# Kernel optimization log

Measured on AMD Instinct MI355X. Metric: run time of the kernel, lower is better.

## Reference

```python
import jax, jax.numpy as jnp
import numpy as np

N, C, H, W = 8, 512, 64, 64
C8, C2 = C // 8, C // 2  # 64, 256


def _maxpool2(x):
    # 2x2 max pool, stride 2. x: [n, c, h, w] -> [n, c, h//2, w//2]
    n, c, h, w = x.shape
    return x.reshape(n, c, h // 2, 2, w // 2, 2).max(axis=(3, 5))


def setup_inputs() -> dict:
    key = jax.random.key(0)
    ks = jax.random.split(key, 6)
    s = lambda fan_in: 1.0 / np.sqrt(fan_in)
    return {
        "x": jax.random.normal(ks[0], (N, C, H, W), dtype=jnp.float32),
        "theta_w": jax.random.normal(ks[1], (C8, C), dtype=jnp.float32) * s(C),
        "theta_b": jnp.zeros((C8,), dtype=jnp.float32),
        "phi_w": jax.random.normal(ks[2], (C8, C), dtype=jnp.float32) * s(C),
        "phi_b": jnp.zeros((C8,), dtype=jnp.float32),
        "g_w": jax.random.normal(ks[3], (C2, C), dtype=jnp.float32) * s(C),
        "g_b": jnp.zeros((C2,), dtype=jnp.float32),
        "out_w": jax.random.normal(ks[4], (C, C2), dtype=jnp.float32) * s(C2),
        "out_b": jnp.zeros((C,), dtype=jnp.float32),
        "gamma": jnp.ones((1,), dtype=jnp.float32),
    }


def reference(x, theta_w, theta_b, phi_w, phi_b, g_w, g_b, out_w, out_b, gamma):
    n, c, h, w = x.shape
    hw, hw4 = h * w, (h * w) // 4

    # 1x1 convs == per-pixel matmuls over channels
    theta = jnp.einsum('nchw,kc->nkhw', x, theta_w) + theta_b[None, :, None, None]
    phi = jnp.einsum('nchw,kc->nkhw', x, phi_w) + phi_b[None, :, None, None]
    g = jnp.einsum('nchw,kc->nkhw', x, g_w) + g_b[None, :, None, None]

    theta = theta.reshape(n, -1, hw).transpose(0, 2, 1)        # [n, hw, c/8]
    phi = _maxpool2(phi).reshape(n, -1, hw4)                    # [n, c/8, hw/4]
    g = _maxpool2(g).reshape(n, -1, hw4)                        # [n, c/2, hw/4]

    energy = jnp.einsum('nqk,nkp->nqp', theta, phi)             # [n, hw, hw/4]
    attention = jax.nn.softmax(energy, axis=-1)

    out = jnp.einsum('ncp,nqp->ncq', g, attention)              # [n, c/2, hw]
    out = out.reshape(n, c // 2, h, w)
    out = jnp.einsum('nchw,kc->nkhw', out, out_w) + out_b[None, :, None, None]
    return gamma[0] * out + x
```

## Files before the change

kernel.cpp:

```cpp
#include <hip/hip_runtime.h>
#include <hip/hip_bf16.h>
#include <cmath>
#include <cstdint>

#define NB 8
#define HW 4096
#define PP 1024
#define C2 256

typedef _Float16 half_t;
typedef _Float16 half8 __attribute__((ext_vector_type(8)));
typedef _Float16 half4 __attribute__((ext_vector_type(4)));
typedef _Float16 half2t __attribute__((ext_vector_type(2)));
typedef float f32x4 __attribute__((ext_vector_type(4)));

__global__ __launch_bounds__(256) void prep_k(
    const float* __restrict__ tw, const float* __restrict__ pw,
    const float* __restrict__ gw, const float* __restrict__ ow,
    half_t* __restrict__ W16,
    const float* __restrict__ x, half_t* __restrict__ x16t)
{
    const int tid = threadIdx.x;
    const int bx = blockIdx.x;

    if (bx < 160) {
        int gid = bx * 256 + tid;
        size_t i0 = (size_t)gid * 8;
        const float* src; size_t off;
        if (i0 < 32768)       { src = tw; off = i0; }
        else if (i0 < 65536)  { src = pw; off = i0 - 32768; }
        else if (i0 < 196608) { src = gw; off = i0 - 65536; }
        else                  { src = ow; off = i0 - 196608; }
        float4 a = *(const float4*)&src[off];
        float4 b = *(const float4*)&src[off + 4];
        half8 h;
        h[0] = (half_t)a.x; h[1] = (half_t)a.y; h[2] = (half_t)a.z; h[3] = (half_t)a.w;
        h[4] = (half_t)b.x; h[5] = (half_t)b.y; h[6] = (half_t)b.z; h[7] = (half_t)b.w;
        *(half8*)&W16[i0] = h;
        return;
    }

    __shared__ half_t U[64][68];
    const int b = bx - 160;
    const int n  = b >> 9;
    const int bxx = b & 511;
    const int c0 = (bxx & 7) * 64;
    const int p0 = (bxx >> 3) * 64;

#pragma unroll
    for (int it = 0; it < 4; ++it) {
        int c = (tid >> 4) + 16 * it;
        int p4 = (tid & 15) * 4;
        float4 v = *(const float4*)&x[((size_t)n * 512 + c0 + c) * HW + p0 + p4];
        half4 h;
        h[0] = (half_t)v.x; h[1] = (half_t)v.y;
        h[2] = (half_t)v.z; h[3] = (half_t)v.w;
        *(half4*)&U[c][p4] = h;
    }
    __syncthreads();
#pragma unroll
    for (int it = 0; it < 2; ++it) {
        int p = (tid >> 3) + 32 * it;
        int ch = (tid & 7) * 8;
        half8 o;
#pragma unroll
        for (int j = 0; j < 8; ++j) o[j] = U[ch + j][p];
        *(half8*)&x16t[((size_t)n * HW + p0 + p) * 512 + c0 + ch] = o;
    }
}

#define SWZ(row, chunk) (((row) << 6) + ((((chunk) ^ ((row) & 7))) << 3))

__global__ __launch_bounds__(256, 3) void proj_k(
    const half_t* __restrict__ W16, const float* __restrict__ theta_b,
    const float* __restrict__ phi_b, const float* __restrict__ g_b,
    const half_t* __restrict__ x16t, half_t* __restrict__ theta16,
    half_t* __restrict__ phi16, half_t* __restrict__ g16)
{
    __shared__ __align__(16) char smem[36864];
    half_t* As = (half_t*)smem;
    half_t* Bs = (half_t*)(smem + 16384);

    const int tid = threadIdx.x;
    const int wave = tid >> 6, lane = tid & 63;
    const int quad = lane >> 4, lq = lane & 15;
    const int wn = (wave & 1) * 64, wm = (wave >> 1) * 64;
    const int n = blockIdx.z;
    const int p0 = blockIdx.x * 128;
    const int ysel = blockIdx.y;

    const half_t* A16 = (ysel == 0) ? W16
                        : (W16 + 65536 + (size_t)(ysel - 1) * 128 * 512);

    const int sr  = lane >> 3;
    const int scl = lane & 7;
    const int scg = scl ^ sr;

    f32x4 acc[4][4];
#pragma unroll
    for (int mt = 0; mt < 4; ++mt)
#pragma unroll
        for (int nt = 0; nt < 4; ++nt)
            acc[mt][nt] = (f32x4){0.f, 0.f, 0.f, 0.f};

    for (int c0 = 0; c0 < 512; c0 += 64) {
#pragma unroll
        for (int i = 0; i < 4; ++i) {
            int rb = (wave << 5) + (i << 3);
            int r = rb + sr;
            __builtin_amdgcn_global_load_lds(
                (const __attribute__((address_space(1))) uint32_t*)
                    &A16[(size_t)r * 512 + c0 + scg * 8],
                (__attribute__((address_space(3))) uint32_t*)&As[rb * 64],
                16, 0, 0);
        }
#pragma unroll
        for (int i = 0; i < 4; ++i) {
            int rb = (wave << 5) + (i << 3);
            int r = rb + sr;
            __builtin_amdgcn_global_load_lds(
                (const __attribute__((address_space(1))) uint32_t*)
                    &x16t[((size_t)n * HW + p0 + r) * 512 + c0 + scg * 8],
                (__attribute__((address_space(3))) uint32_t*)&Bs[rb * 64],
                16, 0, 0);
        }
        __syncthreads();
#pragma unroll
        for (int ks = 0; ks < 2; ++ks) {
            half8 af[4], bf[4];
#pragma unroll
            for (int mt = 0; mt < 4; ++mt)
                af[mt] = *(const half8*)&As[SWZ(wm + mt * 16 + lq, ks * 4 + quad)];
#pragma unroll
            for (int nt = 0; nt < 4; ++nt)
                bf[nt] = *(const half8*)&Bs[SWZ(wn + nt * 16 + lq, ks * 4 + quad)];
#pragma unroll
            for (int mt = 0; mt < 4; ++mt)
#pragma unroll
                for (int nt = 0; nt < 4; ++nt)
                    acc[mt][nt] = __builtin_amdgcn_mfma_f32_16x16x32_f16(
                        af[mt], bf[nt], acc[mt][nt], 0, 0, 0);
        }
        __syncthreads();
    }

    if (ysel == 0) {
        half_t* Cs = (half_t*)smem;
        if (wm == 0) {
#pragma unroll
            for (int mt = 0; mt < 4; ++mt) {
                float4 bv = *(const float4*)&theta_b[mt * 16 + quad * 4];
#pragma unroll
                for (int nt = 0; nt < 4; ++nt) {
                    int q = p0 + wn + nt * 16 + lq;
                    half4 h;
                    h[0] = (half_t)(acc[mt][nt][0] + bv.x);
                    h[1] = (half_t)(acc[mt][nt][1] + bv.y);
                    h[2] = (half_t)(acc[mt][nt][2] + bv.z);
                    h[3] = (half_t)(acc[mt][nt][3] + bv.w);
                    *(half4*)&theta16[((size_t)n * HW + q) * 64 + mt * 16 + quad * 4] = h;
                }
            }
        } else {
#pragma unroll
            for (int mt = 0; mt < 4; ++mt) {
                float4 bv = *(const float4*)&phi_b[mt * 16 + quad * 4];
#pragma unroll
                for (int nt = 0; nt < 4; ++nt) {
                    int col = wn + nt * 16 + lq;
                    int mr = mt * 16 + quad * 4;
                    Cs[(mr + 0) * 136 + col] = (half_t)(acc[mt][nt][0] + bv.x);
                    Cs[(mr + 1) * 136 + col] = (half_t)(acc[mt][nt][1] + bv.y);
                    Cs[(mr + 2) * 136 + col] = (half_t)(acc[mt][nt][2] + bv.z);
                    Cs[(mr + 3) * 136 + col] = (half_t)(acc[mt][nt][3] + bv.w);
                }
            }
        }
        __syncthreads();
        {
            int pw = tid >> 3;
            int kc = (tid & 7) * 8;
            half8 o;
#pragma unroll
            for (int jj = 0; jj < 8; ++jj) {
                int k = kc + jj;
                float v0 = (float)Cs[k * 136 + 2 * pw];
                float v1 = (float)Cs[k * 136 + 2 * pw + 1];
                float v2 = (float)Cs[k * 136 + 64 + 2 * pw];
                float v3 = (float)Cs[k * 136 + 65 + 2 * pw];
                o[jj] = (half_t)fmaxf(fmaxf(v0, v1), fmaxf(v2, v3));
            }
            *(half8*)&phi16[((size_t)n * PP + (p0 >> 7) * 32 + pw) * 64 + kc] = o;
        }
    } else {
        const int m0 = (ysel - 1) * 128;
        half_t* Cs = (half_t*)smem;
#pragma unroll
        for (int mt = 0; mt < 4; ++mt) {
            float4 bv = *(const float4*)&g_b[m0 + wm + mt * 16 + quad * 4];
#pragma unroll
            for (int nt = 0; nt < 4; ++nt) {
                int col = wn + nt * 16 + lq;
                int mr = wm + mt * 16 + quad * 4;
                Cs[(mr + 0) * 136 + col] = (half_t)(acc[mt][nt][0] + bv.x);
                Cs[(mr + 1) * 136 + col] = (half_t)(acc[mt][nt][1] + bv.y);
                Cs[(mr + 2) * 136 + col] = (half_t)(acc[mt][nt][2] + bv.z);
                Cs[(mr + 3) * 136 + col] = (half_t)(acc[mt][nt][3] + bv.w);
            }
        }
        __syncthreads();
#pragma unroll
        for (int i = 0; i < 16; ++i) {
            int m = (tid >> 5) + 8 * i;
            int pw = tid & 31;
            float v0 = (float)Cs[m * 136 + 2 * pw];
            float v1 = (float)Cs[m * 136 + 2 * pw + 1];
            float v2 = (float)Cs[m * 136 + 64 + 2 * pw];
            float v3 = (float)Cs[m * 136 + 65 + 2 * pw];
            g16[((size_t)n * C2 + m0 + m) * PP + (p0 >> 7) * 32 + pw] =
                (half_t)fmaxf(fmaxf(v0, v1), fmaxf(v2, v3));
        }
    }
}

__global__ __launch_bounds__(256, 2) void attn_fused_k(
    const half_t* __restrict__ theta16,
    const half_t* __restrict__ phi16,
    const half_t* __restrict__ g16,
    const half_t* __restrict__ W16o,
    const float* __restrict__ out_b,
    const float* __restrict__ x,
    const float* __restrict__ gam,
    float* __restrict__ outF)
{
    __shared__ half_t P[64][264];
    __shared__ float redM[4][64];
    __shared__ float redS[4][64];
    __shared__ float Ms[64], alpha_s[64], l_s[64], inv_s[64];

    const int tid  = threadIdx.x;
    const int wave = tid >> 6;
    const int lane = tid & 63;
    const int quad = lane >> 4;
    const int lq   = lane & 15;
    const int n  = blockIdx.y;
    const int q0 = blockIdx.x * 64;
    const int cb = wave * 64;

    const half_t* thN  = theta16 + ((size_t)n * HW + q0) * 64;
    const half_t* phiN = phi16 + (size_t)n * PP * 64;
    const half_t* gN   = g16 + (size_t)n * C2 * PP;

    if (tid < 64) { Ms[tid] = -1e30f; l_s[tid] = 0.f; }

    f32x4 acc[4][4];
#pragma unroll
    for (int ct = 0; ct < 4; ++ct)
#pragma unroll
        for (int qt = 0; qt < 4; ++qt)
            acc[ct][qt] = (f32x4){0.f, 0.f, 0.f, 0.f};

    for (int chunk = 0; chunk < 4; ++chunk) {
        const int pch = chunk * 256;

        half8 tb[4][2];
#pragma unroll
        for (int qt = 0; qt < 4; ++qt)
#pragma unroll
            for (int kb = 0; kb < 2; ++kb)
                tb[qt][kb] = *(const half8*)&thN[(size_t)(qt * 16 + lq) * 64 + kb * 32 + quad * 8];

        float mreg[4] = {-1e30f, -1e30f, -1e30f, -1e30f};
#pragma unroll
        for (int pt = 0; pt < 4; ++pt) {
            int pl = wave * 64 + pt * 16;
            const half_t* pr = &phiN[(size_t)(pch + pl + lq) * 64];
            half8 a0 = *(const half8*)&pr[quad * 8];
            half8 a1 = *(const half8*)&pr[32 + quad * 8];
#pragma unroll
            for (int qt = 0; qt < 4; ++qt) {
                f32x4 c = {0.f, 0.f, 0.f, 0.f};
                c = __builtin_amdgcn_mfma_f32_16x16x32_f16(a0, tb[qt][0], c, 0, 0, 0);
                c = __builtin_amdgcn_mfma_f32_16x16x32_f16(a1, tb[qt][1], c, 0, 0, 0);
                mreg[qt] = fmaxf(mreg[qt], fmaxf(fmaxf(c[0], c[1]), fmaxf(c[2], c[3])));
                half2t h0; h0[0] = (half_t)c[0]; h0[1] = (half_t)c[1];
                half2t h1; h1[0] = (half_t)c[2]; h1[1] = (half_t)c[3];
                *(half2t*)&P[qt * 16 + lq][pl + quad * 4]     = h0;
                *(half2t*)&P[qt * 16 + lq][pl + quad * 4 + 2] = h1;
            }
        }
#pragma unroll
        for (int qt = 0; qt < 4; ++qt) {
            float m = mreg[qt];
            m = fmaxf(m, __shfl_xor(m, 16));
            m = fmaxf(m, __shfl_xor(m, 32));
            mreg[qt] = m;
        }
        if (quad == 0) {
#pragma unroll
            for (int qt = 0; qt < 4; ++qt) redM[wave][qt * 16 + lq] = mreg[qt];
        }
        __syncthreads();

        if (tid < 64) {
            float cm = fmaxf(fmaxf(redM[0][tid], redM[1][tid]),
                             fmaxf(redM[2][tid], redM[3][tid]));
            float Mo = Ms[tid];
            float Mn = fmaxf(Mo, cm);
            alpha_s[tid] = __expf(Mo - Mn);
            Ms[tid] = Mn;
        }
        __syncthreads();

        {
            float al[4];
#pragma unroll
            for (int qt = 0; qt < 4; ++qt) al[qt] = alpha_s[qt * 16 + lq];
#pragma unroll
            for (int ct = 0; ct < 4; ++ct)
#pragma unroll
                for (int qt = 0; qt < 4; ++qt)
#pragma unroll
                    for (int r = 0; r < 4; ++r) acc[ct][qt][r] *= al[qt];
        }

        {
            int q = tid & 63, seg = tid >> 6;
            float M = Ms[q];
            float s = 0.f;
#pragma unroll
            for (int j = 0; j < 8; ++j) {
                half8 v = *(const half8*)&P[q][seg * 64 + j * 8];
                half8 o;
#pragma unroll
                for (int e = 0; e < 8; ++e) {
                    float f = __expf((float)v[e] - M);
                    s += f;
                    o[e] = (half_t)f;
                }
                *(half8*)&P[q][seg * 64 + j * 8] = o;
            }
            redS[seg][q] = s;
        }
        __syncthreads();

        if (tid < 64)
            l_s[tid] = l_s[tid] * alpha_s[tid]
                     + redS[0][tid] + redS[1][tid] + redS[2][tid] + redS[3][tid];

#pragma unroll
        for (int kb = 0; kb < 8; ++kb) {
            half8 b[4];
#pragma unroll
            for (int qt = 0; qt < 4; ++qt)
                b[qt] = *(const half8*)&P[qt * 16 + lq][kb * 32 + quad * 8];
#pragma unroll
            for (int ct = 0; ct < 4; ++ct) {
                half8 a = *(const half8*)&gN[(size_t)(cb + ct * 16 + lq) * PP + pch + kb * 32 + quad * 8];
#pragma unroll
                for (int qt = 0; qt < 4; ++qt)
                    acc[ct][qt] = __builtin_amdgcn_mfma_f32_16x16x32_f16(a, b[qt], acc[ct][qt], 0, 0, 0);
            }
        }
        __syncthreads();
    }

    if (tid < 64) inv_s[tid] = 1.0f / l_s[tid];
    __syncthreads();

    {
        float iv[4];
#pragma unroll
        for (int qt = 0; qt < 4; ++qt) iv[qt] = inv_s[qt * 16 + lq];
#pragma unroll
        for (int ct = 0; ct < 4; ++ct) {
#pragma unroll
            for (int qt = 0; qt < 4; ++qt) {
                half2t h0, h1;
                h0[0] = (half_t)(acc[ct][qt][0] * iv[qt]);
                h0[1] = (half_t)(acc[ct][qt][1] * iv[qt]);
                h1[0] = (half_t)(acc[ct][qt][2] * iv[qt]);
                h1[1] = (half_t)(acc[ct][qt][3] * iv[qt]);
                *(half2t*)&P[qt * 16 + lq][cb + ct * 16 + quad * 4]     = h0;
                *(half2t*)&P[qt * 16 + lq][cb + ct * 16 + quad * 4 + 2] = h1;
            }
        }
    }
    __syncthreads();

    const float g0 = gam[0];
#pragma unroll
    for (int pass = 0; pass < 2; ++pass) {
        const int mb = pass * 256 + wave * 64;
        f32x4 acc2[4][4];
#pragma unroll
        for (int mt = 0; mt < 4; ++mt)
#pragma unroll
            for (int qt = 0; qt < 4; ++qt)
                acc2[mt][qt] = (f32x4){0.f, 0.f, 0.f, 0.f};

#pragma unroll
        for (int kb = 0; kb < 8; ++kb) {
            half8 b[4];
#pragma unroll
            for (int qt = 0; qt < 4; ++qt)
                b[qt] = *(const half8*)&P[qt * 16 + lq][kb * 32 + quad * 8];
#pragma unroll
            for (int mt = 0; mt < 4; ++mt) {
                half8 a = *(const half8*)&W16o[(size_t)(mb + mt * 16 + lq) * 256 + kb * 32 + quad * 8];
#pragma unroll
                for (int qt = 0; qt < 4; ++qt)
                    acc2[mt][qt] = __builtin_amdgcn_mfma_f32_16x16x32_f16(a, b[qt], acc2[mt][qt], 0, 0, 0);
            }
        }

#pragma unroll
        for (int mt = 0; mt < 4; ++mt) {
            float4 bv = *(const float4*)&out_b[mb + mt * 16 + quad * 4];
#pragma unroll
            for (int qt = 0; qt < 4; ++qt) {
                int qg = q0 + qt * 16 + lq;
                int m = mb + mt * 16 + quad * 4;
                size_t off = ((size_t)(n * 512 + m)) * HW + qg;
                outF[off]          = g0 * (acc2[mt][qt][0] + bv.x) + x[off];
                outF[off + HW]     = g0 * (acc2[mt][qt][1] + bv.y) + x[off + HW];
                outF[off + 2*HW]   = g0 * (acc2[mt][qt][2] + bv.z) + x[off + 2*HW];
                outF[off + 3*HW]   = g0 * (acc2[mt][qt][3] + bv.w) + x[off + 3*HW];
            }
        }
    }
}

extern "C" void kernel_launch(void* const* d_in, const int* in_sizes, int n_in,
                              void* d_out, int out_size, void* d_ws, size_t ws_size,
                              hipStream_t stream)
{
    const float* x       = (const float*)d_in[0];
    const float* theta_w = (const float*)d_in[1];
    const float* theta_b = (const float*)d_in[2];
    const float* phi_w   = (const float*)d_in[3];
    const float* phi_b   = (const float*)d_in[4];
    const float* g_w     = (const float*)d_in[5];
    const float* g_b     = (const float*)d_in[6];
    const float* out_w   = (const float*)d_in[7];
    const float* out_b   = (const float*)d_in[8];
    const float* gamma   = (const float*)d_in[9];
    float* out = (float*)d_out;

    char* wsb = (char*)d_ws;
    half_t* x16t    = (half_t*)wsb;
    half_t* W16     = (half_t*)(wsb + 33554432);
    half_t* theta16 = (half_t*)(wsb + 34209792);
    half_t* phi16   = (half_t*)(wsb + 38404096);
    half_t* g16     = (half_t*)(wsb + 39452672);

    prep_k<<<160 + 512 * NB, 256, 0, stream>>>(
        theta_w, phi_w, g_w, out_w, W16, x, x16t);
    proj_k<<<dim3(32, 3, NB), 256, 0, stream>>>(
        W16, theta_b, phi_b, g_b, x16t, theta16, phi16, g16);
    attn_fused_k<<<dim3(HW / 64, NB), 256, 0, stream>>>(
        theta16, phi16, g16, W16 + 196608, out_b, x, gamma, out);
}
```

Baseline: 218.1 us.

## Swizzle prep transpose tile, flatten grids with batch-interleaved block order

New measurement: 213.8 us, median of 2. -2.0%, faster.

```diff
diff --git a/kernel.cpp b/kernel.cpp
--- a/kernel.cpp
+++ b/kernel.cpp
@@ -40,9 +40,9 @@
         return;
     }
 
-    __shared__ half_t U[64][68];
+    __shared__ half_t T[64][72];
     const int b = bx - 160;
-    const int n  = b >> 9;
+    const int n   = b >> 9;
     const int bxx = b & 511;
     const int c0 = (bxx & 7) * 64;
     const int p0 = (bxx >> 3) * 64;
@@ -52,26 +52,28 @@
         int c = (tid >> 4) + 16 * it;
         int p4 = (tid & 15) * 4;
         float4 v = *(const float4*)&x[((size_t)n * 512 + c0 + c) * HW + p0 + p4];
-        half4 h;
-        h[0] = (half_t)v.x; h[1] = (half_t)v.y;
-        h[2] = (half_t)v.z; h[3] = (half_t)v.w;
-        *(half4*)&U[c][p4] = h;
+        float vv[4] = {v.x, v.y, v.z, v.w};
+#pragma unroll
+        for (int k = 0; k < 4; ++k) {
+            int row = p4 + k;
+            int chunk = (((c >> 3) + ((row >> 2) & 7)) & 7);
+            T[row][chunk * 8 + (c & 7)] = (half_t)vv[k];
+        }
     }
     __syncthreads();
 #pragma unroll
     for (int it = 0; it < 2; ++it) {
         int p = (tid >> 3) + 32 * it;
         int ch = (tid & 7) * 8;
-        half8 o;
-#pragma unroll
-        for (int j = 0; j < 8; ++j) o[j] = U[ch + j][p];
+        int chunk = (((ch >> 3) + ((p >> 2) & 7)) & 7);
+        half8 o = *(const half8*)&T[p][chunk * 8];
         *(half8*)&x16t[((size_t)n * HW + p0 + p) * 512 + c0 + ch] = o;
     }
 }
 
 #define SWZ(row, chunk) (((row) << 6) + ((((chunk) ^ ((row) & 7))) << 3))
 
-__global__ __launch_bounds__(256, 3) void proj_k(
+__global__ __launch_bounds__(256, 2) void proj_k(
     const half_t* __restrict__ W16, const float* __restrict__ theta_b,
     const float* __restrict__ phi_b, const float* __restrict__ g_b,
     const half_t* __restrict__ x16t, half_t* __restrict__ theta16,
@@ -85,9 +87,12 @@
     const int wave = tid >> 6, lane = tid & 63;
     const int quad = lane >> 4, lq = lane & 15;
     const int wn = (wave & 1) * 64, wm = (wave >> 1) * 64;
-    const int n = blockIdx.z;
-    const int p0 = blockIdx.x * 128;
-    const int ysel = blockIdx.y;
+
+    const int bid  = blockIdx.x;
+    const int n    = bid & 7;
+    const int rest = bid >> 3;
+    const int p0   = (rest & 31) * 128;
+    const int ysel = rest >> 5;
 
     const half_t* A16 = (ysel == 0) ? W16
                         : (W16 + 65536 + (size_t)(ysel - 1) * 128 * 512);
@@ -243,8 +248,8 @@
     const int lane = tid & 63;
     const int quad = lane >> 4;
     const int lq   = lane & 15;
-    const int n  = blockIdx.y;
-    const int q0 = blockIdx.x * 64;
+    const int n  = blockIdx.x & 7;
+    const int q0 = (blockIdx.x >> 3) * 64;
     const int cb = wave * 64;
 
     const half_t* thN  = theta16 + ((size_t)n * HW + q0) * 64;
@@ -456,8 +461,8 @@
 
     prep_k<<<160 + 512 * NB, 256, 0, stream>>>(
         theta_w, phi_w, g_w, out_w, W16, x, x16t);
-    proj_k<<<dim3(32, 3, NB), 256, 0, stream>>>(
+    proj_k<<<768, 256, 0, stream>>>(
         W16, theta_b, phi_b, g_b, x16t, theta16, phi16, g16);
-    attn_fused_k<<<dim3(HW / 64, NB), 256, 0, stream>>>(
+    attn_fused_k<<<512, 256, 0, stream>>>(
         theta16, phi16, g16, W16 + 196608, out_b, x, gamma, out);
 }
```
